# Optimization experiments

Hardware: AMD Instinct MI355X
Metric: run time of the kernel (lower is better)

## Reference

```python
import jax, jax.numpy as jnp
import numpy as np

L, B, N, W, H = 8, 8, 1024, 768, 12
C = W // H  # per-head channel dim = 64


def setup_inputs() -> dict:
    key = jax.random.key(0)
    ks = jax.random.split(key, 5)
    s = 0.02  # init scale for weights
    return {
        "x": jax.random.normal(ks[0], (B, N, W), jnp.float32),
        "Wqkv": jax.random.normal(ks[1], (L, W, 3 * W), jnp.float32) * s,
        "bqkv": jnp.zeros((L, 3 * W), jnp.float32),
        "Wo": jax.random.normal(ks[2], (L, W, W), jnp.float32) * s,
        "bo": jnp.zeros((L, W), jnp.float32),
        "Wfc": jax.random.normal(ks[3], (L, W, 4 * W), jnp.float32) * s,
        "bfc": jnp.zeros((L, 4 * W), jnp.float32),
        "Wpr": jax.random.normal(ks[4], (L, 4 * W, W), jnp.float32) * s,
        "bpr": jnp.zeros((L, W), jnp.float32),
        "g1": jnp.ones((L, W), jnp.float32),
        "b1": jnp.zeros((L, W), jnp.float32),
        "g2": jnp.ones((L, W), jnp.float32),
        "b2": jnp.zeros((L, W), jnp.float32),
    }


def _ln(x, g, b, eps=1e-5):
    m = jnp.mean(x, axis=-1, keepdims=True)
    v = jnp.var(x, axis=-1, keepdims=True)
    return (x - m) * jax.lax.rsqrt(v + eps) * g + b


def reference(x, Wqkv, bqkv, Wo, bo, Wfc, bfc, Wpr, bpr, g1, b1, g2, b2):
    scale = 1.0 / np.sqrt(np.sqrt(C))  # applied to BOTH q and k, as in source

    def block(h, p):
        wqkv, bq, wo, bo_, wfc, bf, wpr, bp, G1, B1, G2, B2 = p
        # --- attention ---
        y = _ln(h, G1, B1)
        qkv = y @ wqkv + bq                       # [B,N,3W]
        qkv = qkv.reshape(B, N, H, 3 * C)         # per-head interleaved q|k|v
        q, k, v = jnp.split(qkv, 3, axis=-1)      # each [B,N,H,C]
        w = jnp.einsum('bthc,bshc->bhts', q * scale, k * scale)
        w = jax.nn.softmax(w.astype(jnp.float32), axis=-1).astype(w.dtype)
        attn = jnp.einsum('bhts,bshc->bthc', w, v).reshape(B, N, W)
        h = h + attn @ wo + bo_
        # --- MLP (exact GELU, matching torch F.gelu default) ---
        y2 = _ln(h, G2, B2)
        h = h + jax.nn.gelu(y2 @ wfc + bf, approximate=False) @ wpr + bp
        return h, None

    out, _ = jax.lax.scan(block, x, (Wqkv, bqkv, Wo, bo, Wfc, bfc, Wpr, bpr, g1, b1, g2, b2))
    return out
```

## Files before the change

### kernel.cpp

```cpp
#include <hip/hip_runtime.h>
#include <hip/hip_bf16.h>
#include <cstdint>
#include <cstddef>


typedef __attribute__((ext_vector_type(8))) short bf16x8;
typedef __attribute__((ext_vector_type(4))) float f32x4;

#define MFMA16(a, b, c) __builtin_amdgcn_mfma_f32_16x16x32_bf16((a), (b), (c), 0, 0, 0)

__device__ __forceinline__ void gld_lds16(const void* g, void* l) {
    __builtin_amdgcn_global_load_lds((const __attribute__((address_space(1))) unsigned int*)g,
                                     (__attribute__((address_space(3))) unsigned int*)l,
                                     16, 0, 0);
}

__device__ __forceinline__ unsigned short f32_to_bf16_bits(float f) {
    unsigned u = __builtin_bit_cast(unsigned, f);
    u += 0x7fffu + ((u >> 16) & 1u);
    return (unsigned short)(u >> 16);
}

__device__ __forceinline__ unsigned pack_bf2(float a, float b) {
    return (unsigned)f32_to_bf16_bits(a) | ((unsigned)f32_to_bf16_bits(b) << 16);
}

__device__ __forceinline__ unsigned cvt_pk_bf16(float lo, float hi) {
    unsigned r;
    asm("v_cvt_pk_bf16_f32 %0, %1, %2" : "=v"(r) : "v"(lo), "v"(hi));
    return r;
}

template <bool RES, bool GELU, bool WF, bool WH>
__global__ __launch_bounds__(256, 2) void gemm_bt(const __hip_bfloat16* __restrict__ A,
                                                  const __hip_bfloat16* __restrict__ Bt,
                                                  const float* __restrict__ bias,
                                                  const float* __restrict__ res,
                                                  float* __restrict__ outf,
                                                  __hip_bfloat16* __restrict__ outh,
                                                  int N, int K) {
    __shared__ __hip_bfloat16 lA[2][128 * 64];
    __shared__ __hip_bfloat16 lB[2][128 * 64];
    const int t = threadIdx.x;
    const int w = t >> 6, l = t & 63;
    const int lr = l & 15, lg = l >> 4;
    const int x7 = lr & 7;
    const int cs0 = (lg ^ x7) << 3;
    const int cs1 = ((4 | lg) ^ x7) << 3;
    const int bid = blockIdx.x;
    const int xcd = bid & 7;
    const int local = bid >> 3;
    const int m0 = (xcd * 8 + (local & 7)) * 128;
    const int n0 = (local >> 3) * 128;
    const int wm = (w & 1) * 64, wn = (w >> 1) * 64;

    const int srow = t >> 3, sslot = t & 7;
    const int sx = (sslot ^ (srow & 7)) << 3;

    f32x4 acc[4][4];
#pragma unroll
    for (int i = 0; i < 4; i++)
#pragma unroll
        for (int j = 0; j < 4; j++) acc[i][j] = (f32x4){0.f, 0.f, 0.f, 0.f};

#define STAGE(buf, kt)                                                        \
    {                                                                         \
        _Pragma("unroll") for (int j = 0; j < 4; j++) {                       \
            const int row = srow + j * 32;                                    \
            const int gcol = (kt) * 64 + sx;                                  \
            gld_lds16(&A[(size_t)(m0 + row) * K + gcol], &lA[buf][(t + j * 256) * 8]); \
            gld_lds16(&Bt[(size_t)(n0 + row) * K + gcol], &lB[buf][(t + j * 256) * 8]); \
        }                                                                     \
    }

    STAGE(0, 0);
    __syncthreads();

    const int NT = K >> 6;
    for (int kt = 0; kt < NT; ++kt) {
        const int cur = kt & 1;
        if (kt + 1 < NT) STAGE(cur ^ 1, kt + 1);
        const __hip_bfloat16* sA = lA[cur];
        const __hip_bfloat16* sB = lB[cur];
        bf16x8 af[4][2], bf[4][2];
#pragma unroll
        for (int mt = 0; mt < 4; mt++) {
            const int ro = (wm + mt * 16 + lr) * 64;
            af[mt][0] = *(const bf16x8*)&sA[ro + cs0];
            af[mt][1] = *(const bf16x8*)&sA[ro + cs1];
        }
#pragma unroll
        for (int nt = 0; nt < 4; nt++) {
            const int ro = (wn + nt * 16 + lr) * 64;
            bf[nt][0] = *(const bf16x8*)&sB[ro + cs0];
            bf[nt][1] = *(const bf16x8*)&sB[ro + cs1];
        }
#pragma unroll
        for (int mt = 0; mt < 4; mt++)
#pragma unroll
            for (int nt = 0; nt < 4; nt++) {
                acc[mt][nt] = MFMA16(af[mt][0], bf[nt][0], acc[mt][nt]);
                acc[mt][nt] = MFMA16(af[mt][1], bf[nt][1], acc[mt][nt]);
            }
        __syncthreads();
    }
#undef STAGE

#pragma unroll
    for (int nt = 0; nt < 4; nt++) {
        const int col = n0 + wn + nt * 16 + lr;
        const float bv = bias[col];
#pragma unroll
        for (int mt = 0; mt < 4; mt++) {
#pragma unroll
            for (int r = 0; r < 4; r++) {
                const int row = m0 + wm + mt * 16 + lg * 4 + r;
                const size_t idx = (size_t)row * N + col;
                float v = acc[mt][nt][r] + bv;
                if (RES) v += res[idx];
                if (GELU) v = 0.5f * v * (1.f + erff(v * 0.70710678118654752f));
                if (WF) outf[idx] = v;
                if (WH) outh[idx] = __float2bfloat16(v);
            }
        }
    }
}

__global__ __launch_bounds__(256) void ln_kernel(const float* __restrict__ h,
                                                 const float* __restrict__ g,
                                                 const float* __restrict__ b,
                                                 __hip_bfloat16* __restrict__ y) {
    const int t = threadIdx.x;
    const int w = t >> 6, l = t & 63;
    const int row = blockIdx.x * 4 + w;
    const float4* hr = (const float4*)(h + (size_t)row * 768);
    const float4* g4 = (const float4*)g;
    const float4* b4 = (const float4*)b;
    float4 x[3];
    float s = 0.f, q = 0.f;
#pragma unroll
    for (int j = 0; j < 3; j++) {
        x[j] = hr[l + j * 64];
        s += x[j].x + x[j].y + x[j].z + x[j].w;
        q += x[j].x * x[j].x + x[j].y * x[j].y + x[j].z * x[j].z + x[j].w * x[j].w;
    }
#pragma unroll
    for (int d = 1; d < 64; d <<= 1) {
        s += __shfl_xor(s, d);
        q += __shfl_xor(q, d);
    }
    const float mean = s * (1.f / 768.f);
    const float var = q * (1.f / 768.f) - mean * mean;
    const float rs = rsqrtf(var + 1e-5f);
    uint2* yr = (uint2*)(y + (size_t)row * 768);
#pragma unroll
    for (int j = 0; j < 3; j++) {
        const float4 gg = g4[l + j * 64], bb = b4[l + j * 64];
        float o0 = (x[j].x - mean) * rs * gg.x + bb.x;
        float o1 = (x[j].y - mean) * rs * gg.y + bb.y;
        float o2 = (x[j].z - mean) * rs * gg.z + bb.z;
        float o3 = (x[j].w - mean) * rs * gg.w + bb.w;
        yr[l + j * 64] = make_uint2(pack_bf2(o0, o1), pack_bf2(o2, o3));
    }
}

__global__ __launch_bounds__(256) void transpose_weights(const float* __restrict__ sq,
                                                         const float* __restrict__ so,
                                                         const float* __restrict__ sf,
                                                         const float* __restrict__ sp,
                                                         __hip_bfloat16* __restrict__ dq,
                                                         __hip_bfloat16* __restrict__ dO,
                                                         __hip_bfloat16* __restrict__ df,
                                                         __hip_bfloat16* __restrict__ dp) {
    const int bid = blockIdx.x;
    const float* src;
    __hip_bfloat16* dst;
    int K, N, tloc;
    if (bid < 1728)      { src = sq; dst = dq; K = 768;  N = 2304; tloc = bid; }
    else if (bid < 2304) { src = so; dst = dO; K = 768;  N = 768;  tloc = bid - 1728; }
    else if (bid < 4608) { src = sf; dst = df; K = 768;  N = 3072; tloc = bid - 2304; }
    else                 { src = sp; dst = dp; K = 3072; N = 768;  tloc = bid - 4608; }
    const int ktiles = K / 32;
    const int k0 = (tloc % ktiles) * 32;
    const int n0 = (tloc / ktiles) * 32;
    const int t = threadIdx.x;
    __shared__ float tile[32][33];
#pragma unroll
    for (int p = 0; p < 4; p++) {
        int rr = p * 8 + (t >> 5);
        tile[rr][t & 31] = src[(size_t)(k0 + rr) * N + n0 + (t & 31)];
    }
    __syncthreads();
#pragma unroll
    for (int p = 0; p < 4; p++) {
        int rr = p * 8 + (t >> 5);
        dst[(size_t)(n0 + rr) * K + k0 + (t & 31)] = __float2bfloat16(tile[t & 31][rr]);
    }
}

__global__ __launch_bounds__(256) void vt_transpose(const short* __restrict__ qkv,
                                                    short* __restrict__ vt) {
    const int bid = blockIdx.x;
    const int bh = bid >> 6, tau = bid & 63;
    const int b = bh / 12, h = bh % 12;
    const int ct = tau >> 5, nt = tau & 31;
    const int n0 = nt * 32, c0 = ct * 32;
    const int t = threadIdx.x;
    __shared__ short tile[32][33];
    const short* base = qkv + (size_t)(b * 1024 + n0) * 2304 + h * 192 + 128 + c0;
#pragma unroll
    for (int p = 0; p < 4; p++) {
        int rr = p * 8 + (t >> 5);
        tile[rr][t & 31] = base[(size_t)rr * 2304 + (t & 31)];
    }
    __syncthreads();
    short* ob = vt + (size_t)((b * 12 + h) * 64 + c0) * 1024 + n0;
#pragma unroll
    for (int p = 0; p < 4; p++) {
        int rr = p * 8 + (t >> 5);
        ob[(size_t)rr * 1024 + (t & 31)] = tile[t & 31][rr];
    }
}

__global__ __launch_bounds__(256) void attn_kernel(const short* __restrict__ qkv,
                                                   const short* __restrict__ vt,
                                                   short* __restrict__ attnout) {
    const int bid = blockIdx.x;
    const int xcd = bid & 7, j = bid >> 3;
    const int bh = xcd * 12 + (j >> 4);
    const int qt = j & 15;
    const int b = bh / 12, hh = bh % 12;
    const int t = threadIdx.x, w = t >> 6, l = t & 63;
    const int lr = l & 15, lg = l >> 4;
    const int x7 = lr & 7;
    __shared__ short lK[64 * 64];
    __shared__ short lV[64 * 64];
    __shared__ short lP[4][16 * 64];
    const int qw = qt * 64 + w * 16;

    bf16x8 bq[2];
#pragma unroll
    for (int ks = 0; ks < 2; ks++)
        bq[ks] = *(const bf16x8*)&qkv[(size_t)(b * 1024 + qw + lr) * 2304 + hh * 192 + ks * 32 + lg * 8];

    int col[2];
    col[0] = (lg ^ x7) * 8;
    col[1] = ((4 | lg) ^ x7) * 8;

    const int c0 = t, c1 = t + 256;
    const int r0 = c0 >> 3, r1 = c1 >> 3;
    const int s0 = (c0 & 7) ^ (r0 & 7), s1 = (c1 & 7) ^ (r1 & 7);
    const short* gK0 = qkv + (size_t)(b * 1024 + r0) * 2304 + hh * 192 + 64 + s0 * 8;
    const short* gK1 = qkv + (size_t)(b * 1024 + r1) * 2304 + hh * 192 + 64 + s1 * 8;
    const short* gV0 = vt + (size_t)((b * 12 + hh) * 64 + r0) * 1024 + s0 * 8;
    const short* gV1 = vt + (size_t)((b * 12 + hh) * 64 + r1) * 1024 + s1 * 8;

    f32x4 o[4];
#pragma unroll
    for (int dt = 0; dt < 4; dt++) o[dt] = (f32x4){0.f, 0.f, 0.f, 0.f};
    const float cexp = 0.125f * 1.44269504088896f;
    float cm = -1.0e30f;
    float lsum = 0.f;

    for (int kt = 0; kt < 16; kt++) {
        const int key0 = kt * 64;
        __syncthreads();
        gld_lds16(gK0 + (size_t)key0 * 2304, &lK[c0 * 8]);
        gld_lds16(gK1 + (size_t)key0 * 2304, &lK[c1 * 8]);
        gld_lds16(gV0 + key0, &lV[c0 * 8]);
        gld_lds16(gV1 + key0, &lV[c1 * 8]);
        __syncthreads();

        f32x4 s[4];
#pragma unroll
        for (int nt = 0; nt < 4; nt++) s[nt] = (f32x4){0.f, 0.f, 0.f, 0.f};
#pragma unroll
        for (int nt = 0; nt < 4; nt++)
#pragma unroll
            for (int ks = 0; ks < 2; ks++) {
                bf16x8 ak = *(const bf16x8*)&lK[(nt * 16 + lr) * 64 + col[ks]];
                s[nt] = MFMA16(ak, bq[ks], s[nt]);
            }

        float mx = s[0][0];
#pragma unroll
        for (int nt = 0; nt < 4; nt++)
#pragma unroll
            for (int r = 0; r < 4; r++) mx = fmaxf(mx, s[nt][r]);
        mx = fmaxf(mx, __shfl_xor(mx, 16));
        mx = fmaxf(mx, __shfl_xor(mx, 32));
        const float tm = mx * cexp;
        if (!__all(tm <= cm + 8.f)) {
            const float cmn = fmaxf(cm, tm);
            const float alpha = exp2f(cm - cmn);
            cm = cmn;
            lsum *= alpha;
            float af[4];
#pragma unroll
            for (int r = 0; r < 4; r++) af[r] = __shfl(alpha, lg * 4 + r);
#pragma unroll
            for (int dt = 0; dt < 4; dt++)
#pragma unroll
                for (int r = 0; r < 4; r++) o[dt][r] *= af[r];
        }
        float ps = 0.f;
#pragma unroll
        for (int nt = 0; nt < 4; nt++)
#pragma unroll
            for (int r = 0; r < 4; r++) {
                float p = exp2f(s[nt][r] * cexp - cm);
                s[nt][r] = p;
                ps += p;
            }
        ps += __shfl_xor(ps, 16);
        ps += __shfl_xor(ps, 32);
        lsum += ps;

#pragma unroll
        for (int nt = 0; nt < 4; nt++) {
            unsigned pk0 = cvt_pk_bf16(s[nt][0], s[nt][1]);
            unsigned pk1 = cvt_pk_bf16(s[nt][2], s[nt][3]);
            const int S = nt * 2 + (lg >> 1);
            *(uint2*)&lP[w][lr * 64 + ((S ^ x7) << 3) + ((lg & 1) << 2)] = make_uint2(pk0, pk1);
        }

#pragma unroll
        for (int kc = 0; kc < 2; kc++) {
            bf16x8 ap = *(const bf16x8*)&lP[w][lr * 64 + col[kc]];
#pragma unroll
            for (int dt = 0; dt < 4; dt++) {
                bf16x8 bv = *(const bf16x8*)&lV[(dt * 16 + lr) * 64 + col[kc]];
                o[dt] = MFMA16(ap, bv, o[dt]);
            }
        }
    }

    float inv[4];
#pragma unroll
    for (int r = 0; r < 4; r++) inv[r] = 1.f / __shfl(lsum, lg * 4 + r);
#pragma unroll
    for (int dt = 0; dt < 4; dt++)
#pragma unroll
        for (int r = 0; r < 4; r++)
            attnout[(size_t)(b * 1024 + qw + lg * 4 + r) * 768 + hh * 64 + dt * 16 + lr] =
                (short)f32_to_bf16_bits(o[dt][r] * inv[r]);
}

extern "C" void kernel_launch(void* const* d_in, const int* in_sizes, int n_in,
                              void* d_out, int out_size, void* d_ws, size_t ws_size,
                              hipStream_t stream) {
    const float* x    = (const float*)d_in[0];
    const float* Wqkv = (const float*)d_in[1];
    const float* bqkv = (const float*)d_in[2];
    const float* Wo   = (const float*)d_in[3];
    const float* bo   = (const float*)d_in[4];
    const float* Wfc  = (const float*)d_in[5];
    const float* bfc  = (const float*)d_in[6];
    const float* Wpr  = (const float*)d_in[7];
    const float* bpr  = (const float*)d_in[8];
    const float* g1   = (const float*)d_in[9];
    const float* b1   = (const float*)d_in[10];
    const float* g2   = (const float*)d_in[11];
    const float* b2   = (const float*)d_in[12];
    float* h = (float*)d_out;

    char* ws = (char*)d_ws;
    size_t off = 0;
    auto alloc = [&](size_t bytes) -> void* {
        void* p = ws + off;
        off += (bytes + 255) & ~(size_t)255;
        return p;
    };
    __hip_bfloat16* tQKV = (__hip_bfloat16*)alloc((size_t)2304 * 768 * 2);
    __hip_bfloat16* tO   = (__hip_bfloat16*)alloc((size_t)768 * 768 * 2);
    __hip_bfloat16* tFC  = (__hip_bfloat16*)alloc((size_t)3072 * 768 * 2);
    __hip_bfloat16* tPR  = (__hip_bfloat16*)alloc((size_t)768 * 3072 * 2);
    __hip_bfloat16* y    = (__hip_bfloat16*)alloc((size_t)8192 * 768 * 2);
    __hip_bfloat16* att  = (__hip_bfloat16*)alloc((size_t)8192 * 768 * 2);
    __hip_bfloat16* vtb  = (__hip_bfloat16*)alloc((size_t)8192 * 768 * 2);
    __hip_bfloat16* big  = (__hip_bfloat16*)alloc((size_t)8192 * 3072 * 2);
    __hip_bfloat16* qkvb = big;
    __hip_bfloat16* fcb  = big;

    hipMemcpyAsync(h, x, (size_t)8 * 1024 * 768 * 4, hipMemcpyDeviceToDevice, stream);

    for (int L = 0; L < 8; L++) {
        const float* wq = Wqkv + (size_t)L * 768 * 2304;
        const float* wo = Wo   + (size_t)L * 768 * 768;
        const float* wf = Wfc  + (size_t)L * 768 * 3072;
        const float* wp = Wpr  + (size_t)L * 3072 * 768;

        transpose_weights<<<6912, 256, 0, stream>>>(wq, wo, wf, wp, tQKV, tO, tFC, tPR);

        ln_kernel<<<2048, 256, 0, stream>>>(h, g1 + L * 768, b1 + L * 768, y);

        gemm_bt<false, false, false, true><<<18 * 64, 256, 0, stream>>>(
            y, tQKV, bqkv + L * 2304, nullptr, nullptr, qkvb, 2304, 768);

        vt_transpose<<<6144, 256, 0, stream>>>((const short*)qkvb, (short*)vtb);

        attn_kernel<<<1536, 256, 0, stream>>>(
            (const short*)qkvb, (const short*)vtb, (short*)att);

        gemm_bt<true, false, true, false><<<6 * 64, 256, 0, stream>>>(
            att, tO, bo + L * 768, h, h, nullptr, 768, 768);

        ln_kernel<<<2048, 256, 0, stream>>>(h, g2 + L * 768, b2 + L * 768, y);

        gemm_bt<false, true, false, true><<<24 * 64, 256, 0, stream>>>(
            y, tFC, bfc + L * 3072, nullptr, nullptr, fcb, 3072, 768);

        gemm_bt<true, false, true, false><<<6 * 64, 256, 0, stream>>>(
            fcb, tPR, bpr + L * 768, h, h, nullptr, 768, 3072);
    }
}
```

Measured before the change: 2.391 ms.

## Prefetch two stages ahead with vmcnt waits in GEMM and attention

Both the GEMM and the attention kernel now keep two tiles in flight through global-to-LDS async loads. Full __syncthreads are replaced by targeted s_waitcnt vmcnt/lgkmcnt waits plus raw barriers. The GEMM issues the load for tile kt+2 into the buffer just read, once its fragments are in registers. Attention double-buffers its K/V LDS tiles so the next block's loads overlap the softmax and MFMA work. This hides global memory latency but depends on exact vmcnt counts matching the number of outstanding loads, and it raises LDS use in attention.

```diff
diff --git a/kernel.cpp b/kernel.cpp
--- a/kernel.cpp
+++ b/kernel.cpp
@@ -74,12 +74,15 @@
     }
 
     STAGE(0, 0);
-    __syncthreads();
+    STAGE(1, 1);
 
     const int NT = K >> 6;
     for (int kt = 0; kt < NT; ++kt) {
         const int cur = kt & 1;
-        if (kt + 1 < NT) STAGE(cur ^ 1, kt + 1);
+        if (kt + 1 < NT) { asm volatile("s_waitcnt vmcnt(8)" ::: "memory"); }
+        else             { asm volatile("s_waitcnt vmcnt(0)" ::: "memory"); }
+        __builtin_amdgcn_s_barrier();
+        __builtin_amdgcn_sched_barrier(0);
         const __hip_bfloat16* sA = lA[cur];
         const __hip_bfloat16* sB = lB[cur];
         bf16x8 af[4][2], bf[4][2];
@@ -95,6 +98,10 @@
             bf[nt][0] = *(const bf16x8*)&sB[ro + cs0];
             bf[nt][1] = *(const bf16x8*)&sB[ro + cs1];
         }
+        asm volatile("s_waitcnt lgkmcnt(0)" ::: "memory");
+        __builtin_amdgcn_sched_barrier(0);
+        __builtin_amdgcn_s_barrier();
+        if (kt + 2 < NT) STAGE(cur, kt + 2);
 #pragma unroll
         for (int mt = 0; mt < 4; mt++)
 #pragma unroll
@@ -102,7 +109,6 @@
                 acc[mt][nt] = MFMA16(af[mt][0], bf[nt][0], acc[mt][nt]);
                 acc[mt][nt] = MFMA16(af[mt][1], bf[nt][1], acc[mt][nt]);
             }
-        __syncthreads();
     }
 #undef STAGE
 
@@ -233,8 +239,8 @@
     const int t = threadIdx.x, w = t >> 6, l = t & 63;
     const int lr = l & 15, lg = l >> 4;
     const int x7 = lr & 7;
-    __shared__ short lK[64 * 64];
-    __shared__ short lV[64 * 64];
+    __shared__ short lK[2][64 * 64];
+    __shared__ short lV[2][64 * 64];
     __shared__ short lP[4][16 * 64];
     const int qw = qt * 64 + w * 16;
 
@@ -255,6 +261,15 @@
     const short* gV0 = vt + (size_t)((b * 12 + hh) * 64 + r0) * 1024 + s0 * 8;
     const short* gV1 = vt + (size_t)((b * 12 + hh) * 64 + r1) * 1024 + s1 * 8;
 
+#define STAGE_KV(buf, kt)                                           \
+    {                                                               \
+        const int key0_ = (kt) * 64;                                \
+        gld_lds16(gK0 + (size_t)key0_ * 2304, &lK[buf][c0 * 8]);    \
+        gld_lds16(gK1 + (size_t)key0_ * 2304, &lK[buf][c1 * 8]);    \
+        gld_lds16(gV0 + key0_, &lV[buf][c0 * 8]);                   \
+        gld_lds16(gV1 + key0_, &lV[buf][c1 * 8]);                   \
+    }
+
     f32x4 o[4];
 #pragma unroll
     for (int dt = 0; dt < 4; dt++) o[dt] = (f32x4){0.f, 0.f, 0.f, 0.f};
@@ -262,14 +277,15 @@
     float cm = -1.0e30f;
     float lsum = 0.f;
 
+    STAGE_KV(0, 0);
+    STAGE_KV(1, 1);
+
     for (int kt = 0; kt < 16; kt++) {
-        const int key0 = kt * 64;
-        __syncthreads();
-        gld_lds16(gK0 + (size_t)key0 * 2304, &lK[c0 * 8]);
-        gld_lds16(gK1 + (size_t)key0 * 2304, &lK[c1 * 8]);
-        gld_lds16(gV0 + key0, &lV[c0 * 8]);
-        gld_lds16(gV1 + key0, &lV[c1 * 8]);
-        __syncthreads();
+        const int cur = kt & 1;
+        if (kt < 15) { asm volatile("s_waitcnt vmcnt(4)" ::: "memory"); }
+        else         { asm volatile("s_waitcnt vmcnt(0)" ::: "memory"); }
+        __builtin_amdgcn_s_barrier();
+        __builtin_amdgcn_sched_barrier(0);
 
         f32x4 s[4];
 #pragma unroll
@@ -278,7 +294,7 @@
         for (int nt = 0; nt < 4; nt++)
 #pragma unroll
             for (int ks = 0; ks < 2; ks++) {
-                bf16x8 ak = *(const bf16x8*)&lK[(nt * 16 + lr) * 64 + col[ks]];
+                bf16x8 ak = *(const bf16x8*)&lK[cur][(nt * 16 + lr) * 64 + col[ks]];
                 s[nt] = MFMA16(ak, bq[ks], s[nt]);
             }
 
@@ -329,11 +345,17 @@
             bf16x8 ap = *(const bf16x8*)&lP[w][lr * 64 + col[kc]];
 #pragma unroll
             for (int dt = 0; dt < 4; dt++) {
-                bf16x8 bv = *(const bf16x8*)&lV[(dt * 16 + lr) * 64 + col[kc]];
+                bf16x8 bv = *(const bf16x8*)&lV[cur][(dt * 16 + lr) * 64 + col[kc]];
                 o[dt] = MFMA16(ap, bv, o[dt]);
             }
         }
-    }
+
+        asm volatile("s_waitcnt lgkmcnt(0)" ::: "memory");
+        __builtin_amdgcn_sched_barrier(0);
+        __builtin_amdgcn_s_barrier();
+        if (kt + 2 < 16) STAGE_KV(cur, kt + 2);
+    }
+#undef STAGE_KV
 
     float inv[4];
 #pragma unroll
```

Result: faster. 2.198 ms (-8.1%).
